# Kernel tuning notes

Hardware: AMD Instinct MI355X
Metric: run time of the kernel (lower is better)

The kernel has to match this reference:

```python
import jax, jax.numpy as jnp
import numpy as np

IOU_THR = 0.5
TOP_K = 10
D_MODEL = 256
BS, NQ = 8, 1000


def _layer_norm(x, g, b, eps=1e-5):
    m = x.mean(-1, keepdims=True)
    v = ((x - m) ** 2).mean(-1, keepdims=True)
    return (x - m) * jax.lax.rsqrt(v + eps) * g + b


def _box_iou(boxes):
    # boxes: [nq, 4] xyxy; pairwise IoU [nq, nq]
    area = (boxes[:, 2] - boxes[:, 0]) * (boxes[:, 3] - boxes[:, 1])
    lt = jnp.maximum(boxes[:, None, :2], boxes[None, :, :2])
    rb = jnp.minimum(boxes[:, None, 2:], boxes[None, :, 2:])
    wh = jnp.clip(rb - lt, 0.0)
    inter = wh[..., 0] * wh[..., 1]
    union = area[:, None] + area[None, :] - inter
    return inter / union


def setup_inputs() -> dict:
    key = jax.random.key(0)
    ks = jax.random.split(key, 16)
    d = D_MODEL
    s = 1.0 / np.sqrt(d)
    tgt = jax.random.normal(ks[0], (BS, NQ, d), dtype=jnp.float32)
    seed_mask = (jax.random.uniform(ks[1], (BS, NQ, 1)) < 0.2).astype(jnp.float32)
    # cxcywh boxes in (0,1) with positive wh
    cxy = jax.random.uniform(ks[2], (BS, NQ, 2), minval=0.1, maxval=0.9)
    wh = jax.random.uniform(ks[3], (BS, NQ, 2), minval=0.05, maxval=0.3)
    pred_boxes = jnp.concatenate([cxy, wh], axis=-1).astype(jnp.float32)
    def lin(k):
        kw, kb = jax.random.split(k)
        return (jax.random.uniform(kw, (d, d), minval=-s, maxval=s, dtype=jnp.float32),
                jax.random.uniform(kb, (d,), minval=-s, maxval=s, dtype=jnp.float32))
    W1, b1 = lin(ks[4]); W2, b2 = lin(ks[5]); W3, b3 = lin(ks[6])
    W4, b4 = lin(ks[7]); W5, b5 = lin(ks[8])
    g2 = jnp.ones((d,), jnp.float32); be2 = jnp.zeros((d,), jnp.float32)
    return {"tgt": tgt, "seed_mask": seed_mask, "pred_boxes": pred_boxes,
            "W1": W1, "b1": b1, "W2": W2, "b2": b2, "g2": g2, "be2": be2,
            "W3": W3, "b3": b3, "W4": W4, "b4": b4, "W5": W5, "b5": b5}


def reference(tgt, seed_mask, pred_boxes, W1, b1, W2, b2, g2, be2, W3, b3, W4, b4, W5, b5):
    bs, nq, d = tgt.shape
    # cxcywh -> xyxy
    cxy, wh = pred_boxes[..., :2], pred_boxes[..., 2:]
    box_xyxy = jnp.concatenate([cxy - 0.5 * wh, cxy + 0.5 * wh], axis=-1)
    ious = jax.vmap(_box_iou)(box_xyxy)                       # [bs,nq,nq]
    attn_mask = ious >= IOU_THR
    neg_mask = 1.0 - seed_mask                                # [bs,nq,1]
    # mask out non-seed columns and seed rows
    overlaps = ious * jnp.swapaxes(seed_mask, 1, 2) * neg_mask  # [bs,nq,nq]
    idx = jnp.argsort(-overlaps, axis=-1)[..., :TOP_K]        # [bs,nq,k]
    nmk = jnp.take_along_axis(
        jnp.broadcast_to(jnp.swapaxes(seed_mask, 1, 2), (bs, nq, nq)), idx, axis=2)
    ious_g = jnp.take_along_axis(overlaps, idx, axis=2)       # [bs,nq,k]
    mk = nmk * (ious_g >= IOU_THR).astype(tgt.dtype)          # [bs,nq,k]
    # id token MLP + layernorm
    id_token = _layer_norm(jax.nn.relu(tgt @ W1 + b1) @ W2 + b2, g2, be2)
    # neighbor gather: [bs,nq,k,d]
    neighbors_id = jax.vmap(lambda t, i: t[i])(id_token, idx)
    id_feature = id_token[:, :, None, :] - neighbors_id
    features = jax.nn.relu(id_feature @ W3 + b3) @ W4 + b4
    cur_tgt = (features * mk[..., None]).max(axis=2)          # [bs,nq,d]
    cur_tgt = tgt + jax.nn.relu(cur_tgt @ W5 + b5) * neg_mask
    return cur_tgt, attn_mask
```

## Files before the change

### kernel.cpp

```cpp
#include <hip/hip_runtime.h>
#include <hip/hip_bf16.h>

#define BSZ   8
#define NQ    1000
#define DM    256
#define MROWS (BSZ*NQ)
#define TOPK  10

typedef __attribute__((ext_vector_type(8))) short short8;
typedef __attribute__((ext_vector_type(4))) float f32x4;
typedef unsigned short u16;

static __device__ __forceinline__ float b2f(u16 u) {
    unsigned int x = ((unsigned int)u) << 16;
    return __uint_as_float(x);
}
static __device__ __forceinline__ u16 f2b(float f) {
    __hip_bfloat16 h = __float2bfloat16(f);
    return *(u16*)&h;
}

__global__ __launch_bounds__(256) void prep_iou_k(
    const float* __restrict__ boxes, const float* __restrict__ seed,
    const float* __restrict__ W1, const float* __restrict__ W2,
    const float* __restrict__ W3, const float* __restrict__ W4,
    const float* __restrict__ W5, u16* __restrict__ WT,
    float* __restrict__ attn, int* __restrict__ cnt,
    int* __restrict__ inc0, int* __restrict__ idxs)
{
#pragma clang fp contract(off)
    if (blockIdx.x < 80) {
        const int m  = blockIdx.x >> 4;
        const int kb = (blockIdx.x & 15) * 16;
        const float* W = (m==0)?W1:(m==1)?W2:(m==2)?W3:(m==3)?W4:W5;
        u16* D = WT + (size_t)m * DM * DM;
        const int t = threadIdx.x;
        u16 tmp[16];
        #pragma unroll
        for (int kk = 0; kk < 16; ++kk)
            tmp[kk] = f2b(W[(size_t)(kb+kk)*DM + t]);
        #pragma unroll
        for (int kk = 0; kk < 16; ++kk)
            D[(size_t)t*DM + kb + kk] = tmp[kk];
        return;
    }

    __shared__ float sv[NQ];
    __shared__ int   sj[NQ];
    __shared__ int   scount;
    const int t   = threadIdx.x;
    const int row = blockIdx.x - 80;
    const int b   = row / NQ;
    if (t == 0) scount = 0;

    const float* bi = boxes + (size_t)row * 4;
    const float icx = bi[0], icy = bi[1], iw = bi[2], ih = bi[3];
    const float ix0 = icx - 0.5f*iw, iy0 = icy - 0.5f*ih;
    const float ix1 = icx + 0.5f*iw, iy1 = icy + 0.5f*ih;
    const float area_i = (ix1-ix0)*(iy1-iy0);
    const float neg_i  = 1.f - seed[row];
    __syncthreads();

    float* arow = attn + (size_t)row * NQ;
    for (int j = t; j < NQ; j += 256) {
        const float* bj = boxes + (size_t)(b*NQ + j) * 4;
        const float cx = bj[0], cy = bj[1], w = bj[2], h = bj[3];
        const float x0 = cx - 0.5f*w, y0 = cy - 0.5f*h;
        const float x1 = cx + 0.5f*w, y1 = cy + 0.5f*h;
        const float area_j = (x1-x0)*(y1-y0);
        const float ltx = fmaxf(ix0, x0), lty = fmaxf(iy0, y0);
        const float rbx = fminf(ix1, x1), rby = fminf(iy1, y1);
        const float wx = fmaxf(rbx-ltx, 0.f), wy = fmaxf(rby-lty, 0.f);
        const float inter = wx*wy;
        const float uni = (area_i + area_j) - inter;
        const float iou = inter / uni;
        arow[j] = (iou >= 0.5f) ? 1.0f : 0.0f;
        const float ov = (iou * seed[b*NQ + j]) * neg_i;
        if (ov >= 0.5f) {
            const int p = atomicAdd(&scount, 1);
            if (p < NQ) { sv[p] = ov; sj[p] = j; }
        }
    }
    __syncthreads();

    if (t == 0) {
        const int n = scount;
        inc0[row] = (n < TOPK) ? 1 : 0;
        if (n <= TOPK) {
            cnt[row] = n;
            for (int k = 0; k < n; ++k) idxs[row*TOPK + k] = b*NQ + sj[k];
        } else {
            float bv[TOPK]; int bj[TOPK];
            #pragma unroll
            for (int k = 0; k < TOPK; ++k) { bv[k] = -1.f; bj[k] = 0x7fffffff; }
            for (int e = 0; e < n; ++e) {
                const float v = sv[e]; const int j = sj[e];
                int w = 0;
                #pragma unroll
                for (int k = 1; k < TOPK; ++k)
                    if (bv[k] < bv[w] || (bv[k] == bv[w] && bj[k] > bj[w])) w = k;
                if (v > bv[w] || (v == bv[w] && j < bj[w])) { bv[w] = v; bj[w] = j; }
            }
            cnt[row] = TOPK;
            for (int k = 0; k < TOPK; ++k) idxs[row*TOPK + k] = b*NQ + bj[k];
        }
    }
}

template<int EPI>
static __device__ __forceinline__ void block_gemm256(
    const u16 (*__restrict__ A)[264], const u16* __restrict__ WT,
    const float* __restrict__ bias, u16 (*__restrict__ OutL)[264],
    u16* __restrict__ OutG, float* __restrict__ OutF,
    const float* __restrict__ tgt, const float* __restrict__ seed,
    int r0, u16 (*__restrict__ W_lds)[72], int t)
{
    const int lane = t & 63, wave = t >> 6;
    const int m = lane & 15, quad = lane >> 4;
    f32x4 acc[4];
    #pragma unroll
    for (int nt = 0; nt < 4; ++nt)
        #pragma unroll
        for (int i = 0; i < 4; ++i) acc[nt][i] = 0.f;
    for (int kc = 0; kc < 4; ++kc) {
        __syncthreads();
        #pragma unroll
        for (int pass = 0; pass < 8; ++pass) {
            const int n = pass*32 + (t >> 3), ko = (t & 7) * 8;
            *(uint4*)&W_lds[n][ko] = *(const uint4*)&WT[(size_t)n*DM + kc*64 + ko];
        }
        __syncthreads();
        #pragma unroll
        for (int ks = 0; ks < 2; ++ks) {
            const short8 a = *(const short8*)&A[m][kc*64 + ks*32 + quad*8];
            #pragma unroll
            for (int nt = 0; nt < 4; ++nt) {
                const int n = wave*64 + nt*16 + m;
                const short8 b = *(const short8*)&W_lds[n][ks*32 + quad*8];
                acc[nt] = __builtin_amdgcn_mfma_f32_16x16x32_bf16(a, b, acc[nt], 0, 0, 0);
            }
        }
    }
    #pragma unroll
    for (int nt = 0; nt < 4; ++nt) {
        const int n = wave*64 + nt*16 + m;
        const float bb = bias ? bias[n] : 0.f;
        #pragma unroll
        for (int reg = 0; reg < 4; ++reg) {
            const int rl = quad*4 + reg;
            float v = acc[nt][reg] + bb;
            if (EPI == 0) OutL[rl][n] = f2b(fmaxf(v, 0.f));
            if (EPI == 1) OutL[rl][n] = f2b(v);
            if (EPI == 2) OutG[(size_t)(r0+rl)*DM + n] = f2b(v);
            if (EPI == 3) {
                const int R = r0 + rl;
                OutF[(size_t)R*DM + n] = tgt[(size_t)R*DM + n]
                                       + fmaxf(v, 0.f) * (1.f - seed[R]);
            }
        }
    }
}

__global__ __launch_bounds__(256) void mlp_k(
    const float* __restrict__ tgt, const u16* __restrict__ WT,
    const float* __restrict__ b1, const float* __restrict__ b2,
    const float* __restrict__ g2, const float* __restrict__ be2,
    u16* __restrict__ P)
{
    __shared__ __align__(16) u16 bufA[16][264];
    __shared__ __align__(16) u16 bufB[16][264];
    __shared__ __align__(16) u16 W_lds[256][72];
    const int t = threadIdx.x, r0 = blockIdx.x * 16;
    const int lane = t & 63, wave = t >> 6;

    {
        const int r = t >> 4, c0 = (t & 15) * 16;
        const float* src = &tgt[(size_t)(r0 + r)*DM + c0];
        u16 h[16];
        #pragma unroll
        for (int q = 0; q < 4; ++q) {
            const float4 f = *(const float4*)&src[q*4];
            h[q*4+0] = f2b(f.x); h[q*4+1] = f2b(f.y);
            h[q*4+2] = f2b(f.z); h[q*4+3] = f2b(f.w);
        }
        *(uint4*)&bufA[r][c0]     = *(uint4*)&h[0];
        *(uint4*)&bufA[r][c0 + 8] = *(uint4*)&h[8];
    }
    const u16* W1T = WT;
    const u16* W2T = WT + (size_t)1*DM*DM;
    const u16* W3T = WT + (size_t)2*DM*DM;

    block_gemm256<0>(bufA, W1T, b1, bufB, nullptr, nullptr, nullptr, nullptr, r0, W_lds, t);
    block_gemm256<1>(bufB, W2T, b2, bufA, nullptr, nullptr, nullptr, nullptr, r0, W_lds, t);
    __syncthreads();
    for (int rr = 0; rr < 4; ++rr) {
        const int row = wave*4 + rr;
        float x[4];
        #pragma unroll
        for (int i = 0; i < 4; ++i) x[i] = b2f(bufA[row][lane + 64*i]);
        float s = x[0]+x[1]+x[2]+x[3];
        float q = x[0]*x[0]+x[1]*x[1]+x[2]*x[2]+x[3]*x[3];
        #pragma unroll
        for (int off = 32; off; off >>= 1) {
            s += __shfl_down(s, off, 64);
            q += __shfl_down(q, off, 64);
        }
        s = __shfl(s, 0, 64); q = __shfl(q, 0, 64);
        const float mn  = s * (1.f/DM);
        const float vr  = q * (1.f/DM) - mn*mn;
        const float inv = rsqrtf(vr + 1e-5f);
        #pragma unroll
        for (int i = 0; i < 4; ++i) {
            const int c = lane + 64*i;
            bufA[row][c] = f2b((x[i]-mn)*inv*g2[c] + be2[c]);
        }
    }
    block_gemm256<2>(bufA, W3T, nullptr, nullptr, P, nullptr, nullptr, nullptr, r0, W_lds, t);
}

__global__ __launch_bounds__(256) void pairs_final_k(
    const u16* __restrict__ P, const u16* __restrict__ WT,
    const float* __restrict__ b3, const float* __restrict__ b4,
    const float* __restrict__ b5,
    const int* __restrict__ cnt, const int* __restrict__ inc0,
    const int* __restrict__ idxs,
    const float* __restrict__ tgt, const float* __restrict__ seed,
    float* __restrict__ out)
{
    __shared__ __align__(16) u16 U[16][264];
    __shared__ __align__(16) u16 W_lds[256][72];
    __shared__ float cm[16][264];
    __shared__ int pl_rl[176], pl_j[176];
    __shared__ int sInc[16];
    __shared__ int np;
    const int t = threadIdx.x, r0 = blockIdx.x * 16;
    const int lane = t & 63, wave = t >> 6;
    const int m = lane & 15, quad = lane >> 4;
    const u16* W4T = WT + (size_t)3*DM*DM;
    const u16* W5T = WT + (size_t)4*DM*DM;

    if (t == 0) np = 0;
    __syncthreads();
    if (t < 16) {
        const int r = r0 + t;
        int c = cnt[r];
        c = (c < 0) ? 0 : ((c > TOPK) ? TOPK : c);
        sInc[t] = inc0[r];
        const int base = atomicAdd(&np, c);
        for (int k = 0; k < c; ++k) {
            pl_rl[base + k] = t;
            int j = idxs[r*TOPK + k];
            j = (j < 0) ? 0 : ((j >= MROWS) ? MROWS-1 : j);
            pl_j[base + k] = j;
        }
    }
    __syncthreads();
    const int npairs = np;
    #pragma unroll
    for (int rl = 0; rl < 16; ++rl)
        cm[rl][t] = sInc[rl] ? 0.f : -3.402823466e38f;

    const float bb3 = b3[t];
    float* Dl = (float*)&W_lds[0][0];

    for (int pc = 0; pc*16 < npairs; ++pc) {
        #pragma unroll
        for (int p = 0; p < 16; ++p) {
            const int pr = pc*16 + p;
            u16 uv = 0;
            if (pr < npairs) {
                const int i = r0 + pl_rl[pr];
                const int j = pl_j[pr];
                const float u = fmaxf(b2f(P[(size_t)i*DM + t]) - b2f(P[(size_t)j*DM + t]) + bb3, 0.f);
                uv = f2b(u);
            }
            U[p][t] = uv;
        }
        f32x4 acc[4];
        #pragma unroll
        for (int nt = 0; nt < 4; ++nt)
            #pragma unroll
            for (int i = 0; i < 4; ++i) acc[nt][i] = 0.f;
        for (int kc = 0; kc < 4; ++kc) {
            __syncthreads();
            #pragma unroll
            for (int pass = 0; pass < 8; ++pass) {
                const int n = pass*32 + (t >> 3), ko = (t & 7) * 8;
                *(uint4*)&W_lds[n][ko] = *(const uint4*)&W4T[(size_t)n*DM + kc*64 + ko];
            }
            __syncthreads();
            #pragma unroll
            for (int ks = 0; ks < 2; ++ks) {
                const short8 a = *(const short8*)&U[m][kc*64 + ks*32 + quad*8];
                #pragma unroll
                for (int nt = 0; nt < 4; ++nt) {
                    const int n = wave*64 + nt*16 + m;
                    const short8 b = *(const short8*)&W_lds[n][ks*32 + quad*8];
                    acc[nt] = __builtin_amdgcn_mfma_f32_16x16x32_bf16(a, b, acc[nt], 0, 0, 0);
                }
            }
        }
        __syncthreads();
        #pragma unroll
        for (int nt = 0; nt < 4; ++nt) {
            const int n = wave*64 + nt*16 + m;
            const float bb4 = b4[n];
            #pragma unroll
            for (int reg = 0; reg < 4; ++reg)
                Dl[(quad*4 + reg)*264 + n] = acc[nt][reg] + bb4;
        }
        __syncthreads();
        #pragma unroll
        for (int p = 0; p < 16; ++p) {
            const int pr = pc*16 + p;
            if (pr < npairs) {
                const int rl = pl_rl[pr];
                cm[rl][t] = fmaxf(cm[rl][t], Dl[p*264 + t]);
            }
        }
    }
    #pragma unroll
    for (int rl = 0; rl < 16; ++rl)
        U[rl][t] = f2b(cm[rl][t]);
    block_gemm256<3>(U, W5T, b5, nullptr, nullptr, out, tgt, seed, r0, W_lds, t);
}

extern "C" void kernel_launch(void* const* d_in, const int* in_sizes, int n_in,
                              void* d_out, int out_size, void* d_ws, size_t ws_size,
                              hipStream_t stream)
{
    (void)in_sizes; (void)n_in; (void)out_size; (void)ws_size;
    const float* tgt   = (const float*)d_in[0];
    const float* seed  = (const float*)d_in[1];
    const float* boxes = (const float*)d_in[2];
    const float* W1 = (const float*)d_in[3];
    const float* b1 = (const float*)d_in[4];
    const float* W2 = (const float*)d_in[5];
    const float* b2 = (const float*)d_in[6];
    const float* g2 = (const float*)d_in[7];
    const float* be2= (const float*)d_in[8];
    const float* W3 = (const float*)d_in[9];
    const float* b3 = (const float*)d_in[10];
    const float* W4 = (const float*)d_in[11];
    const float* b4 = (const float*)d_in[12];
    const float* W5 = (const float*)d_in[13];
    const float* b5 = (const float*)d_in[14];

    float* out_tgt  = (float*)d_out;
    float* out_attn = out_tgt + (size_t)MROWS * DM;

    u16* WT   = (u16*)d_ws;
    u16* P    = WT + (size_t)5*DM*DM;
    int* cnt  = (int*)(P + (size_t)MROWS*DM);
    int* inc0 = cnt + MROWS;
    int* idxs = inc0 + MROWS;

    prep_iou_k<<<80 + MROWS, 256, 0, stream>>>(boxes, seed, W1, W2, W3, W4, W5,
                                               WT, out_attn, cnt, inc0, idxs);
    mlp_k<<<MROWS/16, 256, 0, stream>>>(tgt, WT, b1, b2, g2, be2, P);
    pairs_final_k<<<MROWS/16, 256, 0, stream>>>(P, WT, b3, b4, b5, cnt, inc0, idxs,
                                                tgt, seed, out_tgt);
}
```

Measured before the change: 142.4 us.

## Drop LDS weight staging, use wave-per-row IoU and atomic-max pair reduction

The GEMM helpers now read the bf16 weight tiles straight from global memory (via cache) instead of staging them into LDS with two barriers per k-chunk. The IoU/top-k kernel switches from one block per row with an LDS atomic counter to one wave per row, using ballot/popcount compaction, 16 rows per block and 500 blocks. The pair max-reduction in pairs_final_k uses order-preserving uint encoding with LDS atomicMax instead of a staged float buffer. This cuts barriers and LDS traffic. In exchange the MFMA operands now depend on global-load latency, and top-k still runs serially on lane 0.

```diff
diff --git a/kernel.cpp b/kernel.cpp
--- a/kernel.cpp
+++ b/kernel.cpp
@@ -6,114 +6,34 @@
 #define DM    256
 #define MROWS (BSZ*NQ)
 #define TOPK  10
+#define NBLK  500
 
 typedef __attribute__((ext_vector_type(8))) short short8;
 typedef __attribute__((ext_vector_type(4))) float f32x4;
 typedef unsigned short u16;
-
-static __device__ __forceinline__ float b2f(u16 u) {
-    unsigned int x = ((unsigned int)u) << 16;
-    return __uint_as_float(x);
-}
+typedef unsigned int   u32;
+
+static __device__ __forceinline__ float b2f(u16 u) { return __uint_as_float(((u32)u) << 16); }
 static __device__ __forceinline__ u16 f2b(float f) {
     __hip_bfloat16 h = __float2bfloat16(f);
     return *(u16*)&h;
 }
-
-__global__ __launch_bounds__(256) void prep_iou_k(
-    const float* __restrict__ boxes, const float* __restrict__ seed,
-    const float* __restrict__ W1, const float* __restrict__ W2,
-    const float* __restrict__ W3, const float* __restrict__ W4,
-    const float* __restrict__ W5, u16* __restrict__ WT,
-    float* __restrict__ attn, int* __restrict__ cnt,
-    int* __restrict__ inc0, int* __restrict__ idxs)
-{
-#pragma clang fp contract(off)
-    if (blockIdx.x < 80) {
-        const int m  = blockIdx.x >> 4;
-        const int kb = (blockIdx.x & 15) * 16;
-        const float* W = (m==0)?W1:(m==1)?W2:(m==2)?W3:(m==3)?W4:W5;
-        u16* D = WT + (size_t)m * DM * DM;
-        const int t = threadIdx.x;
-        u16 tmp[16];
-        #pragma unroll
-        for (int kk = 0; kk < 16; ++kk)
-            tmp[kk] = f2b(W[(size_t)(kb+kk)*DM + t]);
-        #pragma unroll
-        for (int kk = 0; kk < 16; ++kk)
-            D[(size_t)t*DM + kb + kk] = tmp[kk];
-        return;
-    }
-
-    __shared__ float sv[NQ];
-    __shared__ int   sj[NQ];
-    __shared__ int   scount;
-    const int t   = threadIdx.x;
-    const int row = blockIdx.x - 80;
-    const int b   = row / NQ;
-    if (t == 0) scount = 0;
-
-    const float* bi = boxes + (size_t)row * 4;
-    const float icx = bi[0], icy = bi[1], iw = bi[2], ih = bi[3];
-    const float ix0 = icx - 0.5f*iw, iy0 = icy - 0.5f*ih;
-    const float ix1 = icx + 0.5f*iw, iy1 = icy + 0.5f*ih;
-    const float area_i = (ix1-ix0)*(iy1-iy0);
-    const float neg_i  = 1.f - seed[row];
-    __syncthreads();
-
-    float* arow = attn + (size_t)row * NQ;
-    for (int j = t; j < NQ; j += 256) {
-        const float* bj = boxes + (size_t)(b*NQ + j) * 4;
-        const float cx = bj[0], cy = bj[1], w = bj[2], h = bj[3];
-        const float x0 = cx - 0.5f*w, y0 = cy - 0.5f*h;
-        const float x1 = cx + 0.5f*w, y1 = cy + 0.5f*h;
-        const float area_j = (x1-x0)*(y1-y0);
-        const float ltx = fmaxf(ix0, x0), lty = fmaxf(iy0, y0);
-        const float rbx = fminf(ix1, x1), rby = fminf(iy1, y1);
-        const float wx = fmaxf(rbx-ltx, 0.f), wy = fmaxf(rby-lty, 0.f);
-        const float inter = wx*wy;
-        const float uni = (area_i + area_j) - inter;
-        const float iou = inter / uni;
-        arow[j] = (iou >= 0.5f) ? 1.0f : 0.0f;
-        const float ov = (iou * seed[b*NQ + j]) * neg_i;
-        if (ov >= 0.5f) {
-            const int p = atomicAdd(&scount, 1);
-            if (p < NQ) { sv[p] = ov; sj[p] = j; }
-        }
-    }
-    __syncthreads();
-
-    if (t == 0) {
-        const int n = scount;
-        inc0[row] = (n < TOPK) ? 1 : 0;
-        if (n <= TOPK) {
-            cnt[row] = n;
-            for (int k = 0; k < n; ++k) idxs[row*TOPK + k] = b*NQ + sj[k];
-        } else {
-            float bv[TOPK]; int bj[TOPK];
-            #pragma unroll
-            for (int k = 0; k < TOPK; ++k) { bv[k] = -1.f; bj[k] = 0x7fffffff; }
-            for (int e = 0; e < n; ++e) {
-                const float v = sv[e]; const int j = sj[e];
-                int w = 0;
-                #pragma unroll
-                for (int k = 1; k < TOPK; ++k)
-                    if (bv[k] < bv[w] || (bv[k] == bv[w] && bj[k] > bj[w])) w = k;
-                if (v > bv[w] || (v == bv[w] && j < bj[w])) { bv[w] = v; bj[w] = j; }
-            }
-            cnt[row] = TOPK;
-            for (int k = 0; k < TOPK; ++k) idxs[row*TOPK + k] = b*NQ + bj[k];
-        }
-    }
+static __device__ __forceinline__ u32 encf(float f) {
+    u32 u = __float_as_uint(f);
+    return (u & 0x80000000u) ? ~u : (u | 0x80000000u);
+}
+static __device__ __forceinline__ float decf(u32 e) {
+    u32 u = (e & 0x80000000u) ? (e ^ 0x80000000u) : ~e;
+    return __uint_as_float(u);
 }
 
 template<int EPI>
-static __device__ __forceinline__ void block_gemm256(
+static __device__ __forceinline__ void gemm16(
     const u16 (*__restrict__ A)[264], const u16* __restrict__ WT,
     const float* __restrict__ bias, u16 (*__restrict__ OutL)[264],
     u16* __restrict__ OutG, float* __restrict__ OutF,
     const float* __restrict__ tgt, const float* __restrict__ seed,
-    int r0, u16 (*__restrict__ W_lds)[72], int t)
+    int r0, int t)
 {
     const int lane = t & 63, wave = t >> 6;
     const int m = lane & 15, quad = lane >> 4;
@@ -122,25 +42,20 @@
     for (int nt = 0; nt < 4; ++nt)
         #pragma unroll
         for (int i = 0; i < 4; ++i) acc[nt][i] = 0.f;
-    for (int kc = 0; kc < 4; ++kc) {
-        __syncthreads();
-        #pragma unroll
-        for (int pass = 0; pass < 8; ++pass) {
-            const int n = pass*32 + (t >> 3), ko = (t & 7) * 8;
-            *(uint4*)&W_lds[n][ko] = *(const uint4*)&WT[(size_t)n*DM + kc*64 + ko];
-        }
-        __syncthreads();
+    __syncthreads();
+    #pragma unroll
+    for (int kc = 0; kc < 4; ++kc)
         #pragma unroll
         for (int ks = 0; ks < 2; ++ks) {
-            const short8 a = *(const short8*)&A[m][kc*64 + ks*32 + quad*8];
+            const int k0 = kc*64 + ks*32 + quad*8;
+            const short8 a = *(const short8*)&A[m][k0];
             #pragma unroll
             for (int nt = 0; nt < 4; ++nt) {
                 const int n = wave*64 + nt*16 + m;
-                const short8 b = *(const short8*)&W_lds[n][ks*32 + quad*8];
+                const short8 b = *(const short8*)&WT[(size_t)n*DM + k0];
                 acc[nt] = __builtin_amdgcn_mfma_f32_16x16x32_bf16(a, b, acc[nt], 0, 0, 0);
             }
         }
-    }
     #pragma unroll
     for (int nt = 0; nt < 4; ++nt) {
         const int n = wave*64 + nt*16 + m;
@@ -161,6 +76,96 @@
     }
 }
 
+__global__ __launch_bounds__(256) void prep_iou_k(
+    const float* __restrict__ boxes, const float* __restrict__ seed,
+    const float* __restrict__ W1, const float* __restrict__ W2,
+    const float* __restrict__ W3, const float* __restrict__ W4,
+    const float* __restrict__ W5, u16* __restrict__ WT,
+    float* __restrict__ attn, int* __restrict__ cnt,
+    int* __restrict__ inc0, int* __restrict__ idxs)
+{
+#pragma clang fp contract(off)
+    __shared__ float sv_s[4][NQ];
+    __shared__ int   sj_s[4][NQ];
+    const int t = threadIdx.x, bl = blockIdx.x;
+    const int lane = t & 63, wave = t >> 6;
+
+    if (bl < 80) {
+        const int mm = bl >> 4;
+        const int kb = (bl & 15) * 16;
+        const float* W = (mm==0)?W1:(mm==1)?W2:(mm==2)?W3:(mm==3)?W4:W5;
+        u16* D = WT + (size_t)mm * DM * DM;
+        u16 tmp[16];
+        #pragma unroll
+        for (int kk = 0; kk < 16; ++kk)
+            tmp[kk] = f2b(W[(size_t)(kb+kk)*DM + t]);
+        #pragma unroll
+        for (int kk = 0; kk < 16; ++kk)
+            D[(size_t)t*DM + kb + kk] = tmp[kk];
+    }
+
+    float* sv = sv_s[wave];
+    int*   sj = sj_s[wave];
+    for (int rr = 0; rr < 4; ++rr) {
+        const int row = bl*16 + wave*4 + rr;
+        const int b   = row / NQ;
+        const float4 bi = *(const float4*)(boxes + (size_t)row * 4);
+        const float ix0 = bi.x - 0.5f*bi.z, iy0 = bi.y - 0.5f*bi.w;
+        const float ix1 = bi.x + 0.5f*bi.z, iy1 = bi.y + 0.5f*bi.w;
+        const float area_i = (ix1-ix0)*(iy1-iy0);
+        const float neg_i  = 1.f - seed[row];
+        float* arow = attn + (size_t)row * NQ;
+        int count = 0;
+        for (int c = 0; c < 16; ++c) {
+            const int j = c*64 + lane;
+            bool pred = false; float ov = 0.f;
+            if (j < NQ) {
+                const float4 bj = *(const float4*)(boxes + (size_t)(b*NQ + j) * 4);
+                const float x0 = bj.x - 0.5f*bj.z, y0 = bj.y - 0.5f*bj.w;
+                const float x1 = bj.x + 0.5f*bj.z, y1 = bj.y + 0.5f*bj.w;
+                const float area_j = (x1-x0)*(y1-y0);
+                const float ltx = fmaxf(ix0, x0), lty = fmaxf(iy0, y0);
+                const float rbx = fminf(ix1, x1), rby = fminf(iy1, y1);
+                const float wx = fmaxf(rbx-ltx, 0.f), wy = fmaxf(rby-lty, 0.f);
+                const float inter = wx*wy;
+                const float uni = (area_i + area_j) - inter;
+                const float iou = inter / uni;
+                arow[j] = (iou >= 0.5f) ? 1.0f : 0.0f;
+                ov = (iou * seed[b*NQ + j]) * neg_i;
+                pred = (ov >= 0.5f);
+            }
+            const unsigned long long mask = __ballot(pred);
+            if (pred) {
+                const int pos = count + __popcll(mask & ((1ull << lane) - 1ull));
+                sv[pos] = ov; sj[pos] = j;
+            }
+            count += (int)__popcll(mask);
+        }
+        if (lane == 0) {
+            const int n = count;
+            inc0[row] = (n < TOPK) ? 1 : 0;
+            if (n <= TOPK) {
+                cnt[row] = n;
+                for (int k = 0; k < n; ++k) idxs[row*TOPK + k] = b*NQ + sj[k];
+            } else {
+                float bv[TOPK]; int bj[TOPK];
+                #pragma unroll
+                for (int k = 0; k < TOPK; ++k) { bv[k] = -1.f; bj[k] = 0x7fffffff; }
+                for (int e = 0; e < n; ++e) {
+                    const float v = sv[e]; const int j = sj[e];
+                    int w = 0;
+                    #pragma unroll
+                    for (int k = 1; k < TOPK; ++k)
+                        if (bv[k] < bv[w] || (bv[k] == bv[w] && bj[k] > bj[w])) w = k;
+                    if (v > bv[w] || (v == bv[w] && j < bj[w])) { bv[w] = v; bj[w] = j; }
+                }
+                cnt[row] = TOPK;
+                for (int k = 0; k < TOPK; ++k) idxs[row*TOPK + k] = b*NQ + bj[k];
+            }
+        }
+    }
+}
+
 __global__ __launch_bounds__(256) void mlp_k(
     const float* __restrict__ tgt, const u16* __restrict__ WT,
     const float* __restrict__ b1, const float* __restrict__ b2,
@@ -169,9 +174,11 @@
 {
     __shared__ __align__(16) u16 bufA[16][264];
     __shared__ __align__(16) u16 bufB[16][264];
-    __shared__ __align__(16) u16 W_lds[256][72];
     const int t = threadIdx.x, r0 = blockIdx.x * 16;
     const int lane = t & 63, wave = t >> 6;
+    const u16* W1T = WT;
+    const u16* W2T = WT + (size_t)1*DM*DM;
+    const u16* W3T = WT + (size_t)2*DM*DM;
 
     {
         const int r = t >> 4, c0 = (t & 15) * 16;
@@ -186,12 +193,8 @@
         *(uint4*)&bufA[r][c0]     = *(uint4*)&h[0];
         *(uint4*)&bufA[r][c0 + 8] = *(uint4*)&h[8];
     }
-    const u16* W1T = WT;
-    const u16* W2T = WT + (size_t)1*DM*DM;
-    const u16* W3T = WT + (size_t)2*DM*DM;
-
-    block_gemm256<0>(bufA, W1T, b1, bufB, nullptr, nullptr, nullptr, nullptr, r0, W_lds, t);
-    block_gemm256<1>(bufB, W2T, b2, bufA, nullptr, nullptr, nullptr, nullptr, r0, W_lds, t);
+    gemm16<0>(bufA, W1T, b1, bufB, nullptr, nullptr, nullptr, nullptr, r0, t);
+    gemm16<1>(bufB, W2T, b2, bufA, nullptr, nullptr, nullptr, nullptr, r0, t);
     __syncthreads();
     for (int rr = 0; rr < 4; ++rr) {
         const int row = wave*4 + rr;
@@ -215,7 +218,7 @@
             bufA[row][c] = f2b((x[i]-mn)*inv*g2[c] + be2[c]);
         }
     }
-    block_gemm256<2>(bufA, W3T, nullptr, nullptr, P, nullptr, nullptr, nullptr, r0, W_lds, t);
+    gemm16<2>(bufA, W3T, nullptr, nullptr, P, nullptr, nullptr, nullptr, r0, t);
 }
 
 __global__ __launch_bounds__(256) void pairs_final_k(
@@ -228,12 +231,11 @@
     float* __restrict__ out)
 {
     __shared__ __align__(16) u16 U[16][264];
-    __shared__ __align__(16) u16 W_lds[256][72];
-    __shared__ float cm[16][264];
+    __shared__ u32 cmU[16][264];
     __shared__ int pl_rl[176], pl_j[176];
     __shared__ int sInc[16];
     __shared__ int np;
-    const int t = threadIdx.x, r0 = blockIdx.x * 16;
+    const int t = threadIdx.x, bl = blockIdx.x, r0 = bl * 16;
     const int lane = t & 63, wave = t >> 6;
     const int m = lane & 15, quad = lane >> 4;
     const u16* W4T = WT + (size_t)3*DM*DM;
@@ -257,72 +259,60 @@
     __syncthreads();
     const int npairs = np;
     #pragma unroll
-    for (int rl = 0; rl < 16; ++rl)
-        cm[rl][t] = sInc[rl] ? 0.f : -3.402823466e38f;
-
+    for (int rl2 = 0; rl2 < 16; ++rl2)
+        cmU[rl2][t] = sInc[rl2] ? 0x80000000u  : encf(-3.402823466e38f);
     const float bb3 = b3[t];
-    float* Dl = (float*)&W_lds[0][0];
 
     for (int pc = 0; pc*16 < npairs; ++pc) {
         #pragma unroll
-        for (int p = 0; p < 16; ++p) {
-            const int pr = pc*16 + p;
+        for (int pp = 0; pp < 16; ++pp) {
+            const int pr = pc*16 + pp;
             u16 uv = 0;
             if (pr < npairs) {
                 const int i = r0 + pl_rl[pr];
                 const int j = pl_j[pr];
-                const float u = fmaxf(b2f(P[(size_t)i*DM + t]) - b2f(P[(size_t)j*DM + t]) + bb3, 0.f);
-                uv = f2b(u);
-            }
-            U[p][t] = uv;
-        }
+                uv = f2b(fmaxf(b2f(P[(size_t)i*DM + t]) - b2f(P[(size_t)j*DM + t]) + bb3, 0.f));
+            }
+            U[pp][t] = uv;
+        }
+        __syncthreads();
         f32x4 acc[4];
         #pragma unroll
         for (int nt = 0; nt < 4; ++nt)
             #pragma unroll
             for (int i = 0; i < 4; ++i) acc[nt][i] = 0.f;
-        for (int kc = 0; kc < 4; ++kc) {
-            __syncthreads();
-            #pragma unroll
-            for (int pass = 0; pass < 8; ++pass) {
-                const int n = pass*32 + (t >> 3), ko = (t & 7) * 8;
-                *(uint4*)&W_lds[n][ko] = *(const uint4*)&W4T[(size_t)n*DM + kc*64 + ko];
-            }
-            __syncthreads();
+        #pragma unroll
+        for (int kc = 0; kc < 4; ++kc)
             #pragma unroll
             for (int ks = 0; ks < 2; ++ks) {
-                const short8 a = *(const short8*)&U[m][kc*64 + ks*32 + quad*8];
+                const int k0 = kc*64 + ks*32 + quad*8;
+                const short8 a = *(const short8*)&U[m][k0];
                 #pragma unroll
                 for (int nt = 0; nt < 4; ++nt) {
                     const int n = wave*64 + nt*16 + m;
-                    const short8 b = *(const short8*)&W_lds[n][ks*32 + quad*8];
+                    const short8 b = *(const short8*)&W4T[(size_t)n*DM + k0];
                     acc[nt] = __builtin_amdgcn_mfma_f32_16x16x32_bf16(a, b, acc[nt], 0, 0, 0);
                 }
             }
-        }
-        __syncthreads();
         #pragma unroll
         for (int nt = 0; nt < 4; ++nt) {
             const int n = wave*64 + nt*16 + m;
             const float bb4 = b4[n];
             #pragma unroll
-            for (int reg = 0; reg < 4; ++reg)
-                Dl[(quad*4 + reg)*264 + n] = acc[nt][reg] + bb4;
+            for (int reg = 0; reg < 4; ++reg) {
+                const int pr = pc*16 + quad*4 + reg;
+                if (pr < npairs) {
+                    const int rl2 = pl_rl[pr];
+                    atomicMax(&cmU[rl2][n], encf(acc[nt][reg] + bb4));
+                }
+            }
         }
         __syncthreads();
-        #pragma unroll
-        for (int p = 0; p < 16; ++p) {
-            const int pr = pc*16 + p;
-            if (pr < npairs) {
-                const int rl = pl_rl[pr];
-                cm[rl][t] = fmaxf(cm[rl][t], Dl[p*264 + t]);
-            }
-        }
-    }
-    #pragma unroll
-    for (int rl = 0; rl < 16; ++rl)
-        U[rl][t] = f2b(cm[rl][t]);
-    block_gemm256<3>(U, W5T, b5, nullptr, nullptr, out, tgt, seed, r0, W_lds, t);
+    }
+    #pragma unroll
+    for (int rl2 = 0; rl2 < 16; ++rl2)
+        U[rl2][t] = f2b(decf(cmU[rl2][t]));
+    gemm16<3>(U, W5T, b5, nullptr, nullptr, out, tgt, seed, r0, t);
 }
 
 extern "C" void kernel_launch(void* const* d_in, const int* in_sizes, int n_in,
@@ -355,9 +345,9 @@
     int* inc0 = cnt + MROWS;
     int* idxs = inc0 + MROWS;
 
-    prep_iou_k<<<80 + MROWS, 256, 0, stream>>>(boxes, seed, W1, W2, W3, W4, W5,
-                                               WT, out_attn, cnt, inc0, idxs);
-    mlp_k<<<MROWS/16, 256, 0, stream>>>(tgt, WT, b1, b2, g2, be2, P);
-    pairs_final_k<<<MROWS/16, 256, 0, stream>>>(P, WT, b3, b4, b5, cnt, inc0, idxs,
-                                                tgt, seed, out_tgt);
-}
+    prep_iou_k<<<NBLK, 256, 0, stream>>>(boxes, seed, W1, W2, W3, W4, W5,
+                                         WT, out_attn, cnt, inc0, idxs);
+    mlp_k<<<NBLK, 256, 0, stream>>>(tgt, WT, b1, b2, g2, be2, P);
+    pairs_final_k<<<NBLK, 256, 0, stream>>>(P, WT, b3, b4, b5, cnt, inc0, idxs,
+                                            tgt, seed, out_tgt);
+}
```

Result: slower. 164.1 us (+15.2%).
